# Kernel tuning notes

Measured on AMD Instinct MI355X. Metric: run time of the kernel, lower is better.

The kernel has to match this reference:

```python
import jax, jax.numpy as jnp
import numpy as np

D_MODEL = 4096
N_HEADS = 32
N_KV_HEADS = 8
HEAD_DIM = D_MODEL // N_HEADS  # 128
SEQ = 2048
BATCH = 1
ROPE_BASE = 10000.0


def build_rope_cache(max_seq_len, head_dim, base=10000.0):
    half = head_dim // 2
    pos = jnp.arange(max_seq_len, dtype=jnp.float32)
    inv_freqs = 1.0 / (base ** (jnp.arange(half, dtype=jnp.float32) / half))
    angles = pos[:, None] * inv_freqs[None, :]  # (S, half)
    return jnp.cos(angles), jnp.sin(angles)


def apply_rope(t, cos, sin):
    # t: (B, H, S, D); cos/sin: (S, D//2) broadcast over batch & heads.
    t_even = t[..., 0::2]
    t_odd = t[..., 1::2]
    c = cos[None, None, :, :]
    s = sin[None, None, :, :]
    rot_even = t_even * c - t_odd * s
    rot_odd = t_even * s + t_odd * c
    # interleave back into even/odd slots
    return jnp.stack([rot_even, rot_odd], axis=-1).reshape(t.shape)


def setup_inputs() -> dict:
    key = jax.random.key(0)
    kx, kq, kk, kv, ko = jax.random.split(key, 5)
    bound = 1.0 / np.sqrt(D_MODEL)
    x = jax.random.normal(kx, (BATCH, SEQ, D_MODEL), dtype=jnp.float32)
    # torch Linear weights: (out_features, in_features)
    wq = jax.random.uniform(kq, (N_HEADS * HEAD_DIM, D_MODEL), minval=-bound, maxval=bound, dtype=jnp.float32)
    wk = jax.random.uniform(kk, (N_KV_HEADS * HEAD_DIM, D_MODEL), minval=-bound, maxval=bound, dtype=jnp.float32)
    wv = jax.random.uniform(kv, (N_KV_HEADS * HEAD_DIM, D_MODEL), minval=-bound, maxval=bound, dtype=jnp.float32)
    wo = jax.random.uniform(ko, (D_MODEL, D_MODEL), minval=-bound, maxval=bound, dtype=jnp.float32)
    attn_mask = jnp.tril(jnp.ones((SEQ, SEQ), dtype=jnp.int32))[None, None, :, :]
    return {"x": x, "wq": wq, "wk": wk, "wv": wv, "wo": wo, "attn_mask": attn_mask}


def reference(x, wq, wk, wv, wo, attn_mask):
    B, S, _ = x.shape
    cos, sin = build_rope_cache(SEQ, HEAD_DIM, ROPE_BASE)
    cos, sin = cos[:S], sin[:S]
    q = (x @ wq.T).reshape(B, S, N_HEADS, HEAD_DIM).transpose(0, 2, 1, 3)      # (B,H,S,D)
    k = (x @ wk.T).reshape(B, S, N_KV_HEADS, HEAD_DIM).transpose(0, 2, 1, 3)   # (B,Hkv,S,D)
    v = (x @ wv.T).reshape(B, S, N_KV_HEADS, HEAD_DIM).transpose(0, 2, 1, 3)
    q = apply_rope(q, cos, sin)
    k = apply_rope(k, cos, sin)
    n_rep = N_HEADS // N_KV_HEADS
    if n_rep > 1:
        k = jnp.repeat(k, n_rep, axis=1)
        v = jnp.repeat(v, n_rep, axis=1)
    scores = jnp.einsum('bhqd,bhkd->bhqk', q, k) / jnp.sqrt(jnp.float32(HEAD_DIM))
    scores = jnp.where(attn_mask == 0, -jnp.inf, scores)
    attn = jax.nn.softmax(scores, axis=-1)
    out = jnp.einsum('bhqk,bhkd->bhqd', attn, v)
    out = out.transpose(0, 2, 1, 3).reshape(B, S, D_MODEL)
    return out @ wo.T
```

## Files before the change

kernel.cpp:

```cpp
#include <hip/hip_runtime.h>
#include <hip/hip_bf16.h>

typedef float f32x4 __attribute__((ext_vector_type(4)));
typedef __bf16 bf16x4 __attribute__((ext_vector_type(4)));
typedef __bf16 bf16x8 __attribute__((ext_vector_type(8)));

__device__ __forceinline__ void gld_lds16(const void* g, void* l) {
  __builtin_amdgcn_global_load_lds((const __attribute__((address_space(1))) void*)g,
                                   (__attribute__((address_space(3))) void*)l, 16, 0, 0);
}

__global__ void cvt_f32_bf16(const float* __restrict__ in, __bf16* __restrict__ out,
                             int n8) {
  int idx = blockIdx.x * blockDim.x + threadIdx.x;
  if (idx >= n8) return;
  f32x4 a = *(const f32x4*)(in + (size_t)idx * 8);
  f32x4 b = *(const f32x4*)(in + (size_t)idx * 8 + 4);
  bf16x8 o;
#pragma unroll
  for (int j = 0; j < 4; ++j) { o[j] = (__bf16)a[j]; o[4 + j] = (__bf16)b[j]; }
  *(bf16x8*)(out + (size_t)idx * 8) = o;
}

__global__ void build_trig(float* __restrict__ trig) {
  int idx = blockIdx.x * blockDim.x + threadIdx.x;
  if (idx >= 2048 * 64) return;
  int i = idx & 63, s = idx >> 6;
  float ang = (float)s * powf(10000.0f, -(float)i * (1.0f / 64.0f));
  float sn, cs;
  sincosf(ang, &sn, &cs);
  trig[idx * 2] = cs;
  trig[idx * 2 + 1] = sn;
}

__global__ void rope_bf16(__bf16* __restrict__ T, const float* __restrict__ trig,
                          int stride, int nh_mask, int nh_shift, float mul, int total) {
  int idx = blockIdx.x * blockDim.x + threadIdx.x;
  if (idx >= total) return;
  int i = idx & 63;
  int h = (idx >> 6) & nh_mask;
  int s = idx >> (6 + nh_shift);
  float cs = trig[(s * 64 + i) * 2];
  float sn = trig[(s * 64 + i) * 2 + 1];
  __bf16* p = T + (size_t)s * stride + h * 128 + 2 * i;
  float e = (float)p[0], o = (float)p[1];
  p[0] = (__bf16)((e * cs - o * sn) * mul);
  p[1] = (__bf16)((e * sn + o * cs) * mul);
}

__global__ __launch_bounds__(256) void transpose_v(const __bf16* __restrict__ KVb,
                                                   __bf16* __restrict__ Vt) {
  __shared__ __bf16 T[64][72];
  const int tid = threadIdx.x;
  const int s0 = blockIdx.x * 64, d0 = blockIdx.y * 64;
  const int r = tid >> 3, c8 = (tid & 7) * 8;
#pragma unroll
  for (int i = 0; i < 2; ++i) {
    int row = i * 32 + r;
    *(bf16x8*)&T[row][c8] = *(const bf16x8*)&KVb[(size_t)(s0 + row) * 2048 + 1024 + d0 + c8];
  }
  __syncthreads();
#pragma unroll
  for (int i = 0; i < 2; ++i) {
    int drow = i * 32 + r;
    bf16x8 o;
#pragma unroll
    for (int j = 0; j < 8; ++j) o[j] = T[c8 + j][drow];
    *(bf16x8*)&Vt[(size_t)(d0 + drow) * 2048 + s0 + c8] = o;
  }
}

template <int BM, int BN, typename OutT>
__global__ __launch_bounds__(256) void gemm_bf16(const __bf16* __restrict__ A,
                                                 const __bf16* __restrict__ B0,
                                                 const __bf16* __restrict__ B1,
                                                 int Nsplit, OutT* __restrict__ C,
                                                 int M, int N, int K) {
  constexpr int MI = BM / 32, NJ = BN / 32;
  constexpr int RA = BM / 32, RB = BN / 32;
  __shared__ __bf16 As[BM * 64] __attribute__((aligned(16)));
  __shared__ __bf16 Bs[BN * 64] __attribute__((aligned(16)));

  const int tid = threadIdx.x;
  const int lane = tid & 63;
  const int w = tid >> 6;
  const int nwg = gridDim.x * gridDim.y;
  const int orig = blockIdx.y * gridDim.x + blockIdx.x;
  const int wgid = (orig & 7) * (nwg >> 3) + (orig >> 3);
  const int m0 = (wgid % gridDim.x) * BM;
  const int n0 = (wgid / gridDim.x) * BN;
  const int li = lane & 15, lg = lane >> 4;

  const __bf16* bsrc[RB];
#pragma unroll
  for (int i = 0; i < RB; ++i) {
    int slot = i * 256 + w * 64 + lane;
    int row = slot >> 3;
    int sch = (slot & 7) ^ (row & 7);
    int n = n0 + row;
    bsrc[i] = (n < Nsplit ? B0 + (size_t)n * K : B1 + (size_t)(n - Nsplit) * K) +
              sch * 8;
  }
  const __bf16* asrc[RA];
#pragma unroll
  for (int i = 0; i < RA; ++i) {
    int slot = i * 256 + w * 64 + lane;
    int row = slot >> 3;
    int sch = (slot & 7) ^ (row & 7);
    asrc[i] = A + (size_t)(m0 + row) * K + sch * 8;
  }

  const int wr = (w >> 1) * (BM / 2);
  const int wc = (w & 1) * (BN / 2);

  f32x4 acc[MI][NJ] = {};

  for (int k0 = 0; k0 < K; k0 += 64) {
    __syncthreads();
#pragma unroll
    for (int i = 0; i < RA; ++i)
      gld_lds16(asrc[i] + k0, &As[(i * 256 + w * 64) * 8]);
#pragma unroll
    for (int i = 0; i < RB; ++i)
      gld_lds16(bsrc[i] + k0, &Bs[(i * 256 + w * 64) * 8]);
    __syncthreads();

#pragma unroll
    for (int u = 0; u < 2; ++u) {
      bf16x8 af[MI], bfr[NJ];
#pragma unroll
      for (int mi = 0; mi < MI; ++mi)
        af[mi] = *(const bf16x8*)&As[(wr + mi * 16 + li) * 64 +
                                     (((u * 4 + lg) ^ (li & 7)) * 8)];
#pragma unroll
      for (int nj = 0; nj < NJ; ++nj)
        bfr[nj] = *(const bf16x8*)&Bs[(wc + nj * 16 + li) * 64 +
                                      (((u * 4 + lg) ^ (li & 7)) * 8)];
#pragma unroll
      for (int mi = 0; mi < MI; ++mi)
#pragma unroll
        for (int nj = 0; nj < NJ; ++nj)
          acc[mi][nj] = __builtin_amdgcn_mfma_f32_16x16x32_bf16(af[mi], bfr[nj],
                                                                acc[mi][nj], 0, 0, 0);
    }
  }

  const int crow = lg * 4;
#pragma unroll
  for (int mi = 0; mi < MI; ++mi)
#pragma unroll
    for (int nj = 0; nj < NJ; ++nj)
#pragma unroll
      for (int r = 0; r < 4; ++r)
        C[(size_t)(m0 + wr + mi * 16 + crow + r) * N + (n0 + wc + nj * 16 + li)] =
            (OutT)acc[mi][nj][r];
}

template <typename OutT>
__global__ __launch_bounds__(512) void gemm_bt8(const __bf16* __restrict__ A,
                                                const __bf16* __restrict__ B,
                                                OutT* __restrict__ C,
                                                int M, int N, int K) {
  __shared__ __bf16 As[2][256 * 64] __attribute__((aligned(16)));
  __shared__ __bf16 Bs[2][128 * 64] __attribute__((aligned(16)));

  const int tid = threadIdx.x;
  const int lane = tid & 63;
  const int w = tid >> 6;
  const int nwg = gridDim.x * gridDim.y;
  const int orig = blockIdx.y * gridDim.x + blockIdx.x;
  const int wgid = (orig & 7) * (nwg >> 3) + (orig >> 3);
  const int m0 = (wgid % gridDim.x) * 256;
  const int n0 = (wgid / gridDim.x) * 128;
  const int li = lane & 15, lg = lane >> 4;

  const __bf16* asrc[4];
#pragma unroll
  for (int i = 0; i < 4; ++i) {
    int slot = i * 512 + tid;
    int row = slot >> 3;
    int sch = (slot & 7) ^ (row & 7);
    asrc[i] = A + (size_t)(m0 + row) * K + sch * 8;
  }
  const __bf16* bsrc[2];
#pragma unroll
  for (int i = 0; i < 2; ++i) {
    int slot = i * 512 + tid;
    int row = slot >> 3;
    int sch = (slot & 7) ^ (row & 7);
    bsrc[i] = B + (size_t)(n0 + row) * K + sch * 8;
  }

  auto stage = [&](int buf, int kt) {
    const int k0 = kt * 64;
#pragma unroll
    for (int i = 0; i < 4; ++i)
      gld_lds16(asrc[i] + k0, &As[buf][(i * 512 + w * 64) * 8]);
#pragma unroll
    for (int i = 0; i < 2; ++i)
      gld_lds16(bsrc[i] + k0, &Bs[buf][(i * 512 + w * 64) * 8]);
  };

  const int wm = (w >> 2) * 128;
  const int wn = (w & 3) * 32;

  f32x4 acc[8][2] = {};
  const int NT = K >> 6;

  stage(0, 0);
  stage(1, 1);
  asm volatile("s_waitcnt vmcnt(6)" ::: "memory");
  __builtin_amdgcn_s_barrier();
  __builtin_amdgcn_sched_barrier(0);

#pragma unroll 1
  for (int t = 0; t < NT; ++t) {
    const int cur = t & 1;

#pragma unroll
    for (int u = 0; u < 2; ++u) {
      const int kc = ((u * 4 + lg) ^ (li & 7)) * 8;
      bf16x8 af[8], bfr[2];
#pragma unroll
      for (int mi = 0; mi < 8; ++mi)
        af[mi] = *(const bf16x8*)&As[cur][(wm + mi * 16 + li) * 64 + kc];
#pragma unroll
      for (int nj = 0; nj < 2; ++nj)
        bfr[nj] = *(const bf16x8*)&Bs[cur][(wn + nj * 16 + li) * 64 + kc];
      __builtin_amdgcn_s_setprio(1);
#pragma unroll
      for (int mi = 0; mi < 8; ++mi)
#pragma unroll
        for (int nj = 0; nj < 2; ++nj)
          acc[mi][nj] = __builtin_amdgcn_mfma_f32_16x16x32_bf16(af[mi], bfr[nj],
                                                                acc[mi][nj], 0, 0, 0);
      __builtin_amdgcn_s_setprio(0);
    }

    __builtin_amdgcn_s_barrier();
    __builtin_amdgcn_sched_barrier(0);

    if (t + 2 < NT) {
      stage(cur, t + 2);
      asm volatile("s_waitcnt vmcnt(6)" ::: "memory");
    } else {
      asm volatile("s_waitcnt vmcnt(0)" ::: "memory");
    }
    __builtin_amdgcn_s_barrier();
    __builtin_amdgcn_sched_barrier(0);
  }

#pragma unroll
  for (int mi = 0; mi < 8; ++mi)
#pragma unroll
    for (int nj = 0; nj < 2; ++nj)
#pragma unroll
      for (int r = 0; r < 4; ++r)
        C[(size_t)(m0 + wm + mi * 16 + lg * 4 + r) * N + (n0 + wn + nj * 16 + li)] =
            (OutT)acc[mi][nj][r];
}

__global__ __launch_bounds__(512) void attn_fwd_v6(const __bf16* __restrict__ Q,
                                                   const __bf16* __restrict__ KVb,
                                                   const __bf16* __restrict__ Vt,
                                                   __bf16* __restrict__ O) {
  const int tid = threadIdx.x;
  const int lane = tid & 63;
  const int w = tid >> 6;
  const int orig = blockIdx.x;
  const int chunk = orig & 7;
  const int wkk = orig >> 3;
  const int h = chunk * 4 + (wkk & 3);
  const int pair = wkk >> 2;
  const int kvh = h >> 2;

  __shared__ __bf16 Ks[2][64 * 128] __attribute__((aligned(16)));
  __shared__ __bf16 Vts[2][128 * 64] __attribute__((aligned(16)));
  __shared__ __bf16 Ps[8][16 * 72] __attribute__((aligned(16)));

  const int li = lane & 15, lg = lane >> 4;

  auto stage_k = [&](int k0, int buf) {
#pragma unroll
    for (int i = 0; i < 2; ++i) {
      int slot = i * 512 + tid;
      int row = slot >> 4;
      int sch = (slot & 15) ^ (row & 7);
      gld_lds16(&KVb[(size_t)(k0 + row) * 2048 + kvh * 128 + sch * 8],
                &Ks[buf][(i * 512 + w * 64) * 8]);
    }
  };
  auto stage_v = [&](int k0, int buf) {
#pragma unroll
    for (int i = 0; i < 2; ++i) {
      int slot = i * 512 + tid;
      int row = slot >> 3;
      int sch = (slot & 7) ^ (row & 7);
      gld_lds16(&Vt[(size_t)(kvh * 128 + row) * 2048 + k0 + sch * 8],
                &Vts[buf][(i * 512 + w * 64) * 8]);
    }
  };

#pragma unroll 1
  for (int pass = 0; pass < 2; ++pass) {
    const int m0 = ((pass == 0) ? (15 - pair) : pair) * 128;
    const int rbase = m0 + w * 16;

    bf16x8 qf[4];
    {
      const __bf16* qrow = Q + (size_t)(rbase + li) * 4096 + h * 128;
#pragma unroll
      for (int kc = 0; kc < 4; ++kc) qf[kc] = *(const bf16x8*)(qrow + kc * 32 + lg * 8);
    }

    f32x4 accO[8] = {};
    float plane = 0.f;

    const int wmax = rbase + 15;
    const int ntile = (m0 + 128) >> 6;

    __builtin_amdgcn_s_barrier();
    stage_v(0, 0);
    stage_k(0, 0);

#pragma unroll 1
    for (int t = 0; t < ntile; ++t) {
      const int k0 = t * 64;
      const int cur = t & 1;

      __builtin_amdgcn_s_barrier();
      const int nk = (t + 1 < ntile) ? k0 + 64 : 0;
      stage_v(nk, cur ^ 1);
      stage_k(nk, cur ^ 1);

      asm volatile("s_waitcnt vmcnt(4)" ::: "memory");
      __builtin_amdgcn_s_barrier();
      __builtin_amdgcn_sched_barrier(0);
      asm volatile("" ::: "memory");

      if (k0 <= wmax) {
        f32x4 s2[4] = {};
        __builtin_amdgcn_s_setprio(1);
#pragma unroll
        for (int nt = 0; nt < 4; ++nt)
#pragma unroll
          for (int kc = 0; kc < 4; ++kc) {
            bf16x8 kf = *(const bf16x8*)&Ks[cur][(li + 16 * nt) * 128 +
                                                (((4 * kc + lg) ^ (li & 7)) * 8)];
            s2[nt] = __builtin_amdgcn_mfma_f32_16x16x32_bf16(kf, qf[kc], s2[nt], 0, 0, 0);
          }
        __builtin_amdgcn_s_setprio(0);

        const int q = rbase + li;
        const bool needmask = (k0 + 63 > rbase);
#pragma unroll
        for (int nt = 0; nt < 4; ++nt) {
          bf16x4 pk;
#pragma unroll
          for (int r = 0; r < 4; ++r) {
            const int key = k0 + 16 * nt + lg * 4 + r;
            float v = s2[nt][r];
            if (needmask && key > q) v = -INFINITY;
            float p = exp2f(v);
            plane += p;
            pk[r] = (__bf16)p;
          }
          *(bf16x4*)&Ps[w][li * 72 + 16 * nt + lg * 4] = pk;
        }
        bf16x8 pa[2];
        pa[0] = *(const bf16x8*)&Ps[w][li * 72 + lg * 8];
        pa[1] = *(const bf16x8*)&Ps[w][li * 72 + 32 + lg * 8];

        __builtin_amdgcn_s_setprio(1);
#pragma unroll
        for (int dt = 0; dt < 8; ++dt)
#pragma unroll
          for (int kc = 0; kc < 2; ++kc) {
            bf16x8 vf = *(const bf16x8*)&Vts[cur][(li + 16 * dt) * 64 +
                                                 (((4 * kc + lg) ^ (li & 7)) * 8)];
            accO[dt] = __builtin_amdgcn_mfma_f32_16x16x32_bf16(pa[kc], vf, accO[dt], 0, 0, 0);
          }
        __builtin_amdgcn_s_setprio(0);
      }
    }

    {
      float sum = plane;
      sum += __shfl_xor(sum, 16);
      sum += __shfl_xor(sum, 32);
      float inv[4];
#pragma unroll
      for (int r = 0; r < 4; ++r) inv[r] = 1.0f / __shfl(sum, lg * 4 + r);
#pragma unroll
      for (int dt = 0; dt < 8; ++dt)
#pragma unroll
        for (int r = 0; r < 4; ++r)
          O[(size_t)(rbase + lg * 4 + r) * 4096 + h * 128 + dt * 16 + li] =
              (__bf16)(accO[dt][r] * inv[r]);
    }
  }
}

extern "C" void kernel_launch(void* const* d_in, const int* in_sizes, int n_in,
                              void* d_out, int out_size, void* d_ws, size_t ws_size,
                              hipStream_t stream) {
  const float* x  = (const float*)d_in[0];
  const float* wq = (const float*)d_in[1];
  const float* wk = (const float*)d_in[2];
  const float* wv = (const float*)d_in[3];
  const float* wo = (const float*)d_in[4];
  float* out = (float*)d_out;

  const int S = 2048, D = 4096;
  char* ws = (char*)d_ws;
  __bf16* xb  = (__bf16*)ws;
  __bf16* Qb  = (__bf16*)(ws + 16777216);
  __bf16* KVb = (__bf16*)(ws + 33554432);
  __bf16* Vt  = (__bf16*)(ws + 41943040);
  __bf16* wb  = (__bf16*)(ws + 46137344);
  float*  trig = (float*)(ws + 79691776);
  __bf16* AOb = xb;

  const float qscale = 0.08838834764831845f * 1.4426950408889634f;

  cvt_f32_bf16<<<(S * D / 8 + 255) / 256, 256, 0, stream>>>(x, xb, S * D / 8);
  cvt_f32_bf16<<<(D * D / 8 + 255) / 256, 256, 0, stream>>>(wq, wb, D * D / 8);
  gemm_bt8<__bf16><<<dim3(8, 32), 512, 0, stream>>>(xb, wb, Qb, S, D, D);

  cvt_f32_bf16<<<(1024 * D / 8 + 255) / 256, 256, 0, stream>>>(wk, wb, 1024 * D / 8);
  cvt_f32_bf16<<<(1024 * D / 8 + 255) / 256, 256, 0, stream>>>(wv, wb + (size_t)1024 * D,
                                                               1024 * D / 8);
  gemm_bf16<64, 128, __bf16><<<dim3(32, 16), 256, 0, stream>>>(
      xb, wb, wb + (size_t)1024 * D, 1024, KVb, S, 2048, D);

  build_trig<<<(2048 * 64 + 255) / 256, 256, 0, stream>>>(trig);
  rope_bf16<<<(S * 32 * 64 + 255) / 256, 256, 0, stream>>>(Qb, trig, 4096, 31, 5,
                                                           qscale, S * 32 * 64);
  rope_bf16<<<(S * 8 * 64 + 255) / 256, 256, 0, stream>>>(KVb, trig, 2048, 7, 3,
                                                          1.0f, S * 8 * 64);
  transpose_v<<<dim3(32, 16), 256, 0, stream>>>(KVb, Vt);

  attn_fwd_v6<<<256, 512, 0, stream>>>(Qb, KVb, Vt, AOb);

  cvt_f32_bf16<<<(D * D / 8 + 255) / 256, 256, 0, stream>>>(wo, wb, D * D / 8);
  gemm_bt8<float><<<dim3(8, 32), 512, 0, stream>>>(AOb, wb, out, S, D, D);
}
```

Baseline: 386.0 us.

## Triple-buffer gemm_bt8 LDS and interleave global loads with MFMA phases

The bf16 GEMM moves from double to triple LDS buffering, so the prefetch of tile t+2 goes into a third buffer and no longer waits for compute on the current buffer. The K-loop is split into four MFMA phases, each preceded by its LDS fragment reads and one or two global_load_lds issues, to spread memory traffic across the compute. This aims to cut the stall at the end of each iteration. In exchange, LDS use rises to 144KB per block and the loop gains extra barriers, which could add sync overhead or hurt occupancy. Past the tail the redundant prefetches reload tile t into an unused buffer rather than being skipped.

```diff
diff --git a/kernel.cpp b/kernel.cpp
--- a/kernel.cpp
+++ b/kernel.cpp
@@ -161,8 +161,8 @@
                                                 const __bf16* __restrict__ B,
                                                 OutT* __restrict__ C,
                                                 int M, int N, int K) {
-  __shared__ __bf16 As[2][256 * 64] __attribute__((aligned(16)));
-  __shared__ __bf16 Bs[2][128 * 64] __attribute__((aligned(16)));
+  __shared__ __bf16 As[3][256 * 64] __attribute__((aligned(16)));
+  __shared__ __bf16 Bs[3][128 * 64] __attribute__((aligned(16)));
 
   const int tid = threadIdx.x;
   const int lane = tid & 63;
@@ -191,61 +191,112 @@
     bsrc[i] = B + (size_t)(n0 + row) * K + sch * 8;
   }
 
-  auto stage = [&](int buf, int kt) {
-    const int k0 = kt * 64;
-#pragma unroll
-    for (int i = 0; i < 4; ++i)
-      gld_lds16(asrc[i] + k0, &As[buf][(i * 512 + w * 64) * 8]);
-#pragma unroll
-    for (int i = 0; i < 2; ++i)
-      gld_lds16(bsrc[i] + k0, &Bs[buf][(i * 512 + w * 64) * 8]);
-  };
-
   const int wm = (w >> 2) * 128;
   const int wn = (w & 3) * 32;
 
   f32x4 acc[8][2] = {};
   const int NT = K >> 6;
 
-  stage(0, 0);
-  stage(1, 1);
+#pragma unroll
+  for (int i = 0; i < 4; ++i) gld_lds16(asrc[i], &As[0][(i * 512 + w * 64) * 8]);
+#pragma unroll
+  for (int i = 0; i < 2; ++i) gld_lds16(bsrc[i], &Bs[0][(i * 512 + w * 64) * 8]);
+#pragma unroll
+  for (int i = 0; i < 4; ++i) gld_lds16(asrc[i] + 64, &As[1][(i * 512 + w * 64) * 8]);
+#pragma unroll
+  for (int i = 0; i < 2; ++i) gld_lds16(bsrc[i] + 64, &Bs[1][(i * 512 + w * 64) * 8]);
   asm volatile("s_waitcnt vmcnt(6)" ::: "memory");
   __builtin_amdgcn_s_barrier();
   __builtin_amdgcn_sched_barrier(0);
 
 #pragma unroll 1
   for (int t = 0; t < NT; ++t) {
-    const int cur = t & 1;
-
-#pragma unroll
-    for (int u = 0; u < 2; ++u) {
-      const int kc = ((u * 4 + lg) ^ (li & 7)) * 8;
-      bf16x8 af[8], bfr[2];
-#pragma unroll
-      for (int mi = 0; mi < 8; ++mi)
-        af[mi] = *(const bf16x8*)&As[cur][(wm + mi * 16 + li) * 64 + kc];
+    const int cb = t % 3;
+    const int nb = (t + 2) % 3;
+    const long koff = (long)((t + 2 < NT) ? t + 2 : t) * 64;
+    const __bf16* Asc = &As[cb][0];
+    const __bf16* Bsc = &Bs[cb][0];
+    const int kc0 = (lg ^ (li & 7)) * 8;
+    const int kc1 = ((4 + lg) ^ (li & 7)) * 8;
+
+    bf16x8 af[4], bu[2];
+
+#pragma unroll
+    for (int mi = 0; mi < 4; ++mi)
+      af[mi] = *(const bf16x8*)&Asc[(wm + mi * 16 + li) * 64 + kc0];
+#pragma unroll
+    for (int nj = 0; nj < 2; ++nj)
+      bu[nj] = *(const bf16x8*)&Bsc[(wn + nj * 16 + li) * 64 + kc0];
+    gld_lds16(asrc[0] + koff, &As[nb][(0 * 512 + w * 64) * 8]);
+    gld_lds16(asrc[1] + koff, &As[nb][(1 * 512 + w * 64) * 8]);
+    __builtin_amdgcn_s_barrier();
+    asm volatile("s_waitcnt lgkmcnt(0)" ::: "memory");
+    __builtin_amdgcn_sched_barrier(0);
+    __builtin_amdgcn_s_setprio(1);
+#pragma unroll
+    for (int mi = 0; mi < 4; ++mi)
 #pragma unroll
       for (int nj = 0; nj < 2; ++nj)
-        bfr[nj] = *(const bf16x8*)&Bs[cur][(wn + nj * 16 + li) * 64 + kc];
-      __builtin_amdgcn_s_setprio(1);
-#pragma unroll
-      for (int mi = 0; mi < 8; ++mi)
-#pragma unroll
-        for (int nj = 0; nj < 2; ++nj)
-          acc[mi][nj] = __builtin_amdgcn_mfma_f32_16x16x32_bf16(af[mi], bfr[nj],
-                                                                acc[mi][nj], 0, 0, 0);
-      __builtin_amdgcn_s_setprio(0);
-    }
-
-    __builtin_amdgcn_s_barrier();
+        acc[mi][nj] = __builtin_amdgcn_mfma_f32_16x16x32_bf16(af[mi], bu[nj],
+                                                              acc[mi][nj], 0, 0, 0);
+    __builtin_amdgcn_s_setprio(0);
+    __builtin_amdgcn_s_barrier();
+
+#pragma unroll
+    for (int mi = 0; mi < 4; ++mi)
+      af[mi] = *(const bf16x8*)&Asc[(wm + 64 + mi * 16 + li) * 64 + kc0];
+    gld_lds16(asrc[2] + koff, &As[nb][(2 * 512 + w * 64) * 8]);
+    gld_lds16(asrc[3] + koff, &As[nb][(3 * 512 + w * 64) * 8]);
+    __builtin_amdgcn_s_barrier();
+    asm volatile("s_waitcnt lgkmcnt(0)" ::: "memory");
     __builtin_amdgcn_sched_barrier(0);
-
-    if (t + 2 < NT) {
-      stage(cur, t + 2);
-      asm volatile("s_waitcnt vmcnt(6)" ::: "memory");
-    } else {
-      asm volatile("s_waitcnt vmcnt(0)" ::: "memory");
-    }
+    __builtin_amdgcn_s_setprio(1);
+#pragma unroll
+    for (int mi = 0; mi < 4; ++mi)
+#pragma unroll
+      for (int nj = 0; nj < 2; ++nj)
+        acc[4 + mi][nj] = __builtin_amdgcn_mfma_f32_16x16x32_bf16(af[mi], bu[nj],
+                                                                  acc[4 + mi][nj], 0, 0, 0);
+    __builtin_amdgcn_s_setprio(0);
+    __builtin_amdgcn_s_barrier();
+
+#pragma unroll
+    for (int mi = 0; mi < 4; ++mi)
+      af[mi] = *(const bf16x8*)&Asc[(wm + mi * 16 + li) * 64 + kc1];
+#pragma unroll
+    for (int nj = 0; nj < 2; ++nj)
+      bu[nj] = *(const bf16x8*)&Bsc[(wn + nj * 16 + li) * 64 + kc1];
+    gld_lds16(bsrc[0] + koff, &Bs[nb][(0 * 512 + w * 64) * 8]);
+    __builtin_amdgcn_s_barrier();
+    asm volatile("s_waitcnt lgkmcnt(0)" ::: "memory");
+    __builtin_amdgcn_sched_barrier(0);
+    __builtin_amdgcn_s_setprio(1);
+#pragma unroll
+    for (int mi = 0; mi < 4; ++mi)
+#pragma unroll
+      for (int nj = 0; nj < 2; ++nj)
+        acc[mi][nj] = __builtin_amdgcn_mfma_f32_16x16x32_bf16(af[mi], bu[nj],
+                                                              acc[mi][nj], 0, 0, 0);
+    __builtin_amdgcn_s_setprio(0);
+    __builtin_amdgcn_s_barrier();
+
+#pragma unroll
+    for (int mi = 0; mi < 4; ++mi)
+      af[mi] = *(const bf16x8*)&Asc[(wm + 64 + mi * 16 + li) * 64 + kc1];
+    gld_lds16(bsrc[1] + koff, &Bs[nb][(1 * 512 + w * 64) * 8]);
+    __builtin_amdgcn_s_barrier();
+    asm volatile("s_waitcnt lgkmcnt(0)" ::: "memory");
+    __builtin_amdgcn_sched_barrier(0);
+    __builtin_amdgcn_s_setprio(1);
+#pragma unroll
+    for (int mi = 0; mi < 4; ++mi)
+#pragma unroll
+      for (int nj = 0; nj < 2; ++nj)
+        acc[4 + mi][nj] = __builtin_amdgcn_mfma_f32_16x16x32_bf16(af[mi], bu[nj],
+                                                                  acc[4 + mi][nj], 0, 0, 0);
+    __builtin_amdgcn_s_setprio(0);
+
+    asm volatile("s_waitcnt vmcnt(6)" ::: "memory");
     __builtin_amdgcn_s_barrier();
     __builtin_amdgcn_sched_barrier(0);
   }
```

After: 401.9 us. 1.04x slower.
